# Kernel tuning notes

Hardware: AMD Instinct MI355X
Metric: run time of the kernel (lower is better)

Reference implementation:

```python
import jax, jax.numpy as jnp
import numpy as np

B, C, H, W = 4, 64, 224, 224
WS = 14
HEADS = 4
HD = C // HEADS  # 16
N = WS * WS      # 196
SCALE = HD ** -0.5


def conv2d(x, w, b, pad):
    y = jax.lax.conv_general_dilated(x, w, (1, 1), [(pad, pad), (pad, pad)],
                                     dimension_numbers=('NCHW', 'OIHW', 'NCHW'))
    return y + b[None, :, None, None]


def layernorm(x, g, b, eps=1e-5):
    m = jnp.mean(x, axis=-1, keepdims=True)
    v = jnp.mean((x - m) ** 2, axis=-1, keepdims=True)
    return (x - m) * jax.lax.rsqrt(v + eps) * g + b


def window_partition(x):
    # x: (B,H,W,C) -> (B*nW, WS, WS, C)
    b, h, w, c = x.shape
    x = x.reshape(b, h // WS, WS, w // WS, WS, c)
    return x.transpose(0, 1, 3, 2, 4, 5).reshape(-1, WS, WS, c)


def window_reverse(win, h, w):
    b = win.shape[0] // ((h // WS) * (w // WS))
    x = win.reshape(b, h // WS, w // WS, WS, WS, -1)
    return x.transpose(0, 1, 3, 2, 4, 5).reshape(b, h, w, -1)


def setup_inputs():
    key = jax.random.key(0)
    ks = iter(jax.random.split(key, 64))
    nrm = lambda shp, s=0.02: (jax.random.normal(next(ks), shp, jnp.float32) * s)
    d = {}
    d['x'] = jax.random.normal(next(ks), (B, C, H, W), jnp.float32)
    d['x_basic'] = jax.random.normal(next(ks), (B, C, H, W), jnp.float32)
    # Aware_offset convs
    d['c1_w'] = nrm((64, 64, 3, 3)); d['c1_b'] = jnp.zeros((64,), jnp.float32)
    d['c2_w'] = nrm((64, 64, 5, 5)); d['c2_b'] = jnp.zeros((64,), jnp.float32)
    d['c3_w'] = nrm((64, 64, 7, 7)); d['c3_b'] = jnp.zeros((64,), jnp.float32)
    d['c4_w'] = nrm((64, 192, 3, 3)); d['c4_b'] = jnp.zeros((64,), jnp.float32)
    d['c5_w'] = nrm((128, 128, 3, 3)); d['c5_b'] = jnp.zeros((128,), jnp.float32)
    d['c6_w'] = nrm((128, 128, 3, 3)); d['c6_b'] = jnp.zeros((128,), jnp.float32)
    d['c7_w'] = nrm((64, 128, 1, 1)); d['c7_b'] = jnp.zeros((64,), jnp.float32)
    d['c8_w'] = nrm((64, 128, 1, 1)); d['c8_b'] = jnp.zeros((64,), jnp.float32)
    # block params
    d['qkv1_w'] = nrm((64, 64, 3, 3)); d['qkv1_b'] = jnp.zeros((64,), jnp.float32)
    d['n1_g'] = jnp.ones((C,), jnp.float32); d['n1_b'] = jnp.zeros((C,), jnp.float32)
    d['qkv_w'] = nrm((3 * C, C)); d['qkv_b'] = jnp.zeros((3 * C,), jnp.float32)
    d['corr_w'] = nrm((N, HD)); d['corr_b'] = jnp.zeros((N,), jnp.float32)
    d['proj_w'] = nrm((C, C)); d['proj_b'] = jnp.zeros((C,), jnp.float32)
    d['n2_g'] = jnp.ones((C,), jnp.float32); d['n2_b'] = jnp.zeros((C,), jnp.float32)
    d['fc1_w'] = nrm((2 * C, C)); d['fc1_b'] = jnp.zeros((2 * C,), jnp.float32)
    d['fc2_w'] = nrm((C, 2 * C)); d['fc2_b'] = jnp.zeros((C,), jnp.float32)
    return d


def _forward(x, x_basic, c1_w, c1_b, c2_w, c2_b, c3_w, c3_b, c4_w, c4_b,
             c5_w, c5_b, c6_w, c6_b, c7_w, c7_b, c8_w, c8_b,
             qkv1_w, qkv1_b, n1_g, n1_b, qkv_w, qkv_b, corr_w, corr_b,
             proj_w, proj_b, n2_g, n2_b, fc1_w, fc1_b, fc2_w, fc2_b):
    relu = jax.nn.relu
    # ---- Aware_offset ----
    in1 = relu(conv2d(x, c1_w, c1_b, 1))
    in2 = relu(conv2d(x, c2_w, c2_b, 2))
    in3 = relu(conv2d(x, c3_w, c3_b, 3))
    xo = relu(conv2d(jnp.concatenate([in1, in2, in3], 1), c4_w, c4_b, 1))
    cat12 = jnp.concatenate([x, x_basic], 1)
    b1 = relu(conv2d(cat12, c5_w, c5_b, 1))
    b2 = jax.nn.sigmoid(relu(conv2d(b1, c6_w, c6_b, 1)))
    b1 = relu(conv2d(b1 * b2, c7_w, c7_b, 0))
    xb = xo * b1 + relu(conv2d(cat12, c8_w, c8_b, 0))  # (B,C,H,W)
    xb = xb.transpose(0, 2, 3, 1)                       # (B,H,W,C)
    # ---- pre-attn: norm1 + convQKV1 ----
    xt = x.reshape(B, C, H * W).transpose(0, 2, 1)      # (B,L,C)
    xt = layernorm(xt, n1_g, n1_b)
    xc = xt.reshape(B, H, W, C).transpose(0, 3, 1, 2)
    xc = conv2d(xc, qkv1_w, qkv1_b, 1).transpose(0, 2, 3, 1)  # (B,H,W,C)
    # ---- windows ----
    xw = window_partition(xc).reshape(-1, N, C)   # (B_,N,C)
    xbw = window_partition(xb).reshape(-1, N, C)
    B_ = xw.shape[0]
    # ---- window attention with correction bias ----
    qkv = (xw @ qkv_w.T + qkv_b).reshape(B_, N, 3, HEADS, HD).transpose(2, 0, 3, 1, 4)
    q, k, v = qkv[0] * SCALE, qkv[1], qkv[2]            # (B_,h,N,hd)
    xcorr = xbw.reshape(B_, N, HEADS, HD).transpose(0, 2, 1, 3)
    xcorr = xcorr @ corr_w.T + corr_b                   # (B_,h,N,196)
    attn = jax.nn.softmax(jnp.einsum('bhnd,bhmd->bhnm', q, k) + xcorr, axis=-1)
    out = jnp.einsum('bhnm,bhmd->bhnd', attn, v).transpose(0, 2, 1, 3).reshape(B_, N, C)
    out = out @ proj_w.T + proj_b
    # ---- reverse + MLP ----
    sx = window_reverse(out.reshape(-1, WS, WS, C), H, W)  # (B,H,W,C)
    xt = sx.reshape(B, H * W, C)
    h = layernorm(xt, n2_g, n2_b)
    h = jax.nn.gelu(h @ fc1_w.T + fc1_b, approximate=False) @ fc2_w.T + fc2_b
    xt = xt + h
    return xt.reshape(B, H, W, C).transpose(0, 3, 1, 2)


def reference(x, x_basic, c1_w, c1_b, c2_w, c2_b, c3_w, c3_b, c4_w, c4_b,
              c5_w, c5_b, c6_w, c6_b, c7_w, c7_b, c8_w, c8_b,
              qkv1_w, qkv1_b, n1_g, n1_b, qkv_w, qkv_b, corr_w, corr_b,
              proj_w, proj_b, n2_g, n2_b, fc1_w, fc1_b, fc2_w, fc2_b):
    return _forward(x, x_basic, c1_w, c1_b, c2_w, c2_b, c3_w, c3_b, c4_w, c4_b,
                    c5_w, c5_b, c6_w, c6_b, c7_w, c7_b, c8_w, c8_b,
                    qkv1_w, qkv1_b, n1_g, n1_b, qkv_w, qkv_b, corr_w, corr_b,
                    proj_w, proj_b, n2_g, n2_b, fc1_w, fc1_b, fc2_w, fc2_b)
```

## Files before the change

### kernel.cpp

```cpp
#include <hip/hip_runtime.h>
#include <hip/hip_bf16.h>
#include <math.h>


#define HW  50176
#define WID 224

typedef unsigned short ushortT;
typedef __attribute__((ext_vector_type(8))) short bf8_t;
typedef __attribute__((ext_vector_type(4))) short bf4_t;
typedef __attribute__((ext_vector_type(4))) float f4_t;

__device__ __forceinline__ ushortT f2bf(float v) {
    __hip_bfloat16 h = __float2bfloat16(v);
    ushortT u; __builtin_memcpy(&u, &h, 2); return u;
}
__device__ __forceinline__ float bf2f(ushortT h) {
    union { float f; unsigned int u; } c; c.u = ((unsigned int)h) << 16;
    return c.f;
}
__device__ __forceinline__ void cvt8(const float* xv, bf8_t& hh, bf8_t& ll) {
    #pragma unroll
    for (int i = 0; i < 8; ++i) {
        ushortT hi = f2bf(xv[i]);
        hh[i] = (short)hi;
        ll[i] = (short)f2bf(xv[i] - bf2f(hi));
    }
}

__global__ __launch_bounds__(256) void packw(
    const float* __restrict__ w, ushortT* __restrict__ dst,
    int K, int IC, int OC, int total)
{
    int e = blockIdx.x * 256 + threadIdx.x;
    if (e >= total) return;
    int KK = K * K;
    int kk = e % KK; int rem = e / KK;
    int ic = rem % IC; int oc = rem / IC;
    float v = w[e];
    ushortT hi = f2bf(v);
    ushortT lo = f2bf(v - bf2f(hi));
    int g = oc >> 6, oc64 = oc & 63;
    int ic32 = ic >> 5, icin = ic & 31, kb = icin >> 3, ii = icin & 7;
    int nch = KK * (IC / 32);
    int chunk = ic32 * KK + kk;
    size_t base = ((size_t)(g * nch + chunk)) * 4096;
    dst[base + (kb * 64 + oc64) * 8 + ii] = hi;
    dst[base + 2048 + (kb * 64 + oc64) * 8 + ii] = lo;
}

__global__ __launch_bounds__(256) void packa32(
    const float* __restrict__ w, ushortT* __restrict__ dst, int K, int total)
{
    int e = blockIdx.x * 256 + threadIdx.x;
    if (e >= total) return;
    int f = e >> 9, r = e & 511, ln = r >> 3, i = r & 7;
    int nk = K >> 5;
    int o = f / nk, ks = f % nk;
    int c = ln & 15, gg = ln >> 4;
    float v = w[(size_t)(o * 16 + c) * K + ks * 32 + gg * 8 + i];
    ushortT hi = f2bf(v);
    dst[(size_t)f * 1024 + ln * 8 + i] = hi;
    dst[(size_t)f * 1024 + 512 + ln * 8 + i] = f2bf(v - bf2f(hi));
}

__global__ __launch_bounds__(256) void packa16(
    const float* __restrict__ w, ushortT* __restrict__ dst, int K, int total)
{
    int e = blockIdx.x * 256 + threadIdx.x;
    if (e >= total) return;
    int f = e >> 8, r = e & 255, ln = r >> 2, i = r & 3;
    int nk = K >> 4;
    int o = f / nk, n = f % nk;
    int c = ln & 15, gg = ln >> 4;
    float v = w[(size_t)(o * 16 + c) * K + n * 16 + gg * 4 + i];
    ushortT hi = f2bf(v);
    dst[(size_t)f * 512 + ln * 4 + i] = hi;
    dst[(size_t)f * 512 + 256 + ln * 4 + i] = f2bf(v - bf2f(hi));
}

template<int K>
__device__ __forceinline__ void convpass(
    const ushortT* __restrict__ wq, const ushortT* __restrict__ sm,
    int wv, int lc, int kb, f4_t (&ac)[2][4])
{
    constexpr int off = 3 - K / 2;
    constexpr int INSH = 14 * 22 * 40;
    const int boff = (kb * 64 + lc) * 8;
    bf8_t bh[4], bl[4];
    #pragma unroll
    for (int n = 0; n < 4; ++n) {
        bh[n] = *(const bf8_t*)(wq + boff + n * 128);
        bl[n] = *(const bf8_t*)(wq + 2048 + boff + n * 128);
    }
    #pragma unroll 1
    for (int kk = 0; kk < K * K; ++kk) {
        bf8_t cbh[4], cbl[4];
        #pragma unroll
        for (int n = 0; n < 4; ++n) { cbh[n] = bh[n]; cbl[n] = bl[n]; }
        if (kk + 1 < K * K) {
            const ushortT* wn = wq + (size_t)(kk + 1) * 4096;
            #pragma unroll
            for (int n = 0; n < 4; ++n) {
                bh[n] = *(const bf8_t*)(wn + boff + n * 128);
                bl[n] = *(const bf8_t*)(wn + 2048 + boff + n * 128);
            }
        }
        const int ky = kk / K, kx = kk % K;
        #pragma unroll
        for (int m = 0; m < 2; ++m) {
            const int row = 2 * wv + m + ky + off;
            const int col = lc + kx + off;
            const ushortT* ab = sm + (row * 22 + col) * 40 + kb * 8;
            bf8_t Ah = *(const bf8_t*)ab;
            bf8_t Al = *(const bf8_t*)(ab + INSH);
            #pragma unroll
            for (int n = 0; n < 4; ++n) {
                ac[m][n] = __builtin_amdgcn_mfma_f32_16x16x32_bf16(Ah, cbh[n], ac[m][n], 0, 0, 0);
                ac[m][n] = __builtin_amdgcn_mfma_f32_16x16x32_bf16(Ah, cbl[n], ac[m][n], 0, 0, 0);
                ac[m][n] = __builtin_amdgcn_mfma_f32_16x16x32_bf16(Al, cbh[n], ac[m][n], 0, 0, 0);
            }
        }
    }
}

__global__ __launch_bounds__(256, 4) void mfconv3(
    const float* __restrict__ in,
    const ushortT* __restrict__ w1p, const ushortT* __restrict__ w2p,
    const ushortT* __restrict__ w3p,
    const float* __restrict__ b1, const float* __restrict__ b2,
    const float* __restrict__ b3,
    float* __restrict__ out, int inStride, int outStride)
{
    constexpr int TWd = 22, THd = 14, ICP = 40;
    constexpr int INSH = THd * TWd * ICP;
    constexpr int E = THd * TWd * 32;
    __shared__ __align__(16) ushortT smem_u[2 * INSH];
    float* pool = (float*)smem_u;

    const int t = threadIdx.x, lane = t & 63, wv = t >> 6;
    const int lc = lane & 15, kb = lane >> 4;
    const int img = blockIdx.z;
    const int x0 = blockIdx.x * 16, y0 = blockIdx.y * 8;
    const float* inb = in + (size_t)img * inStride;

    f4_t acc1[2][4], acc2[2][4], acc3[2][4];
    {
        #pragma unroll
        for (int n = 0; n < 4; ++n) {
            float z1 = b1[n * 16 + lc], z2 = b2[n * 16 + lc], z3 = b3[n * 16 + lc];
            #pragma unroll
            for (int m = 0; m < 2; ++m) {
                acc1[m][n] = (f4_t){z1, z1, z1, z1};
                acc2[m][n] = (f4_t){z2, z2, z2, z2};
                acc3[m][n] = (f4_t){z3, z3, z3, z3};
            }
        }
    }

    #pragma unroll 1
    for (int ic32 = 0; ic32 < 2; ++ic32) {
        __syncthreads();
        #pragma unroll 1
        for (int ib = 0; ib < E; ib += 1024) {
            float v[4];
            #pragma unroll
            for (int u = 0; u < 4; ++u) {
                int i = ib + u * 256 + t;
                v[u] = 0.f;
                if (i < E) {
                    int icn = i / (THd * TWd);
                    int px  = i % (THd * TWd);
                    int ty = px / TWd, tx = px % TWd;
                    int gy = y0 + ty - 3, gx = x0 + tx - 3;
                    if (gy >= 0 && gy < WID && gx >= 0 && gx < WID)
                        v[u] = inb[(size_t)(ic32 * 32 + icn) * HW + gy * WID + gx];
                }
            }
            #pragma unroll
            for (int u = 0; u < 4; ++u) {
                int i = ib + u * 256 + t;
                if (i < E) {
                    int icn = i / (THd * TWd);
                    int px  = i % (THd * TWd);
                    ushortT hi = f2bf(v[u]);
                    smem_u[px * ICP + icn] = hi;
                    smem_u[INSH + px * ICP + icn] = f2bf(v[u] - bf2f(hi));
                }
            }
        }
        __syncthreads();
        convpass<3>(w1p + (size_t)(ic32 *  9) * 4096, smem_u, wv, lc, kb, acc1);
        convpass<5>(w2p + (size_t)(ic32 * 25) * 4096, smem_u, wv, lc, kb, acc2);
        convpass<7>(w3p + (size_t)(ic32 * 49) * 4096, smem_u, wv, lc, kb, acc3);
    }

    #pragma unroll 1
    for (int c = 0; c < 3; ++c) {
        float* ob0 = out + (size_t)img * outStride + (size_t)(c * 64) * HW;
        #pragma unroll
        for (int m = 0; m < 2; ++m) {
            __syncthreads();
            #pragma unroll
            for (int n = 0; n < 4; ++n)
                #pragma unroll
                for (int j = 0; j < 4; ++j) {
                    float v = (c == 0) ? acc1[m][n][j] : (c == 1) ? acc2[m][n][j] : acc3[m][n][j];
                    v = fmaxf(v, 0.f);
                    pool[(wv * 64 + n * 16 + lc) * 20 + kb * 4 + j] = v;
                }
            __syncthreads();
            {
                int rho = t >> 6, oc = t & 63;
                int y = y0 + 2 * rho + m;
                float* ob = ob0 + (size_t)oc * HW + (size_t)y * WID + x0;
                const float* pr = &pool[(rho * 64 + oc) * 20];
                #pragma unroll
                for (int c4 = 0; c4 < 4; ++c4) {
                    float4 st = { pr[c4*4+0], pr[c4*4+1], pr[c4*4+2], pr[c4*4+3] };
                    *(float4*)&ob[c4 * 4] = st;
                }
            }
        }
    }
}

template<int K, int IC, int OC, int ACT, bool CAT, bool LNRM, bool NHWCOUT>
__global__ __launch_bounds__(256, 4) void mfconv(
    const float* __restrict__ in, const float* __restrict__ in2,
    const ushortT* __restrict__ wpk, const float* __restrict__ bias,
    const float* __restrict__ mu, const float* __restrict__ rs,
    const float* __restrict__ lng, const float* __restrict__ lnb,
    float* __restrict__ out, int inStride, int outStride)
{
    constexpr int P = K / 2, TWd = 16 + K - 1, THd = 8 + K - 1, ICP = 40;
    constexpr int OCG = OC / 64, KK = K * K, NCH = KK * (IC / 32);
    constexpr int INSH = THd * TWd * ICP;
    constexpr int E = THd * TWd * 32;
    constexpr int SMU = (2 * INSH > 10240) ? 2 * INSH : 10240;
    __shared__ __align__(16) ushortT smem_u[SMU];
    float* pool = (float*)smem_u;

    const int t = threadIdx.x, lane = t & 63, wv = t >> 6;
    const int lc = lane & 15, kb = lane >> 4;
    const int img = blockIdx.z / OCG, g = blockIdx.z % OCG;
    const int x0 = blockIdx.x * 16, y0 = blockIdx.y * 8;
    const float* inb  = in + (size_t)img * inStride;
    const float* in2b = CAT ? (in2 + (size_t)img * inStride) : nullptr;
    const int imgPixBase = img * HW;
    const ushortT* wq0 = wpk + (size_t)g * NCH * 4096;

    f4_t acc[2][4];
    {
        float bz0 = bias[g * 64 +  0 + lc];
        float bz1 = bias[g * 64 + 16 + lc];
        float bz2 = bias[g * 64 + 32 + lc];
        float bz3 = bias[g * 64 + 48 + lc];
        #pragma unroll
        for (int m = 0; m < 2; ++m) {
            acc[m][0] = (f4_t){bz0, bz0, bz0, bz0};
            acc[m][1] = (f4_t){bz1, bz1, bz1, bz1};
            acc[m][2] = (f4_t){bz2, bz2, bz2, bz2};
            acc[m][3] = (f4_t){bz3, bz3, bz3, bz3};
        }
    }
    const int aoff = lc * ICP + kb * 8;
    const int boff = (kb * 64 + lc) * 8;

    #pragma unroll 1
    for (int ic32 = 0; ic32 < IC / 32; ++ic32) {
        __syncthreads();
        #pragma unroll 1
        for (int ib = 0; ib < E; ib += 1024) {
            float v[4];
            #pragma unroll
            for (int u = 0; u < 4; ++u) {
                int i = ib + u * 256 + t;
                v[u] = 0.f;
                if (i < E) {
                    int icn = i / (THd * TWd);
                    int px  = i % (THd * TWd);
                    int ty = px / TWd, tx = px % TWd;
                    int gy = y0 + ty - P, gx = x0 + tx - P;
                    int ic = ic32 * 32 + icn;
                    if (gy >= 0 && gy < WID && gx >= 0 && gx < WID) {
                        const float* s;
                        if (CAT) s = (ic < 64) ? (inb + (size_t)ic * HW)
                                               : (in2b + (size_t)(ic - 64) * HW);
                        else     s = inb + (size_t)ic * HW;
                        float vv = s[gy * WID + gx];
                        if (LNRM) {
                            int p = imgPixBase + gy * WID + gx;
                            vv = (vv - mu[p]) * rs[p] * lng[ic] + lnb[ic];
                        }
                        v[u] = vv;
                    }
                }
            }
            #pragma unroll
            for (int u = 0; u < 4; ++u) {
                int i = ib + u * 256 + t;
                if (i < E) {
                    int icn = i / (THd * TWd);
                    int px  = i % (THd * TWd);
                    ushortT hi = f2bf(v[u]);
                    smem_u[px * ICP + icn] = hi;
                    smem_u[INSH + px * ICP + icn] = f2bf(v[u] - bf2f(hi));
                }
            }
        }
        __syncthreads();
        const ushortT* wqb = wq0 + (size_t)(ic32 * KK) * 4096;
        bf8_t bh[4], bl[4];
        #pragma unroll
        for (int n = 0; n < 4; ++n) {
            bh[n] = *(const bf8_t*)(wqb + boff + n * 128);
            bl[n] = *(const bf8_t*)(wqb + 2048 + boff + n * 128);
        }
        #pragma unroll 1
        for (int kk = 0; kk < KK; ++kk) {
            bf8_t cbh[4], cbl[4];
            #pragma unroll
            for (int n = 0; n < 4; ++n) { cbh[n] = bh[n]; cbl[n] = bl[n]; }
            if (kk + 1 < KK) {
                const ushortT* wn = wqb + (size_t)(kk + 1) * 4096;
                #pragma unroll
                for (int n = 0; n < 4; ++n) {
                    bh[n] = *(const bf8_t*)(wn + boff + n * 128);
                    bl[n] = *(const bf8_t*)(wn + 2048 + boff + n * 128);
                }
            }
            const int ky = kk / K, kx = kk % K;
            #pragma unroll
            for (int m = 0; m < 2; ++m) {
                const int row = 2 * wv + m + ky;
                const ushortT* ab = smem_u + (row * TWd + kx) * ICP + aoff;
                bf8_t Ah = *(const bf8_t*)ab;
                bf8_t Al = *(const bf8_t*)(ab + INSH);
                #pragma unroll
                for (int n = 0; n < 4; ++n) {
                    acc[m][n] = __builtin_amdgcn_mfma_f32_16x16x32_bf16(Ah, cbh[n], acc[m][n], 0, 0, 0);
                    acc[m][n] = __builtin_amdgcn_mfma_f32_16x16x32_bf16(Ah, cbl[n], acc[m][n], 0, 0, 0);
                    acc[m][n] = __builtin_amdgcn_mfma_f32_16x16x32_bf16(Al, cbh[n], acc[m][n], 0, 0, 0);
                }
            }
        }
    }
    if (NHWCOUT) {
        float* ob0 = out + (size_t)img * outStride;
        #pragma unroll
        for (int m = 0; m < 2; ++m) {
            __syncthreads();
            #pragma unroll
            for (int n = 0; n < 4; ++n)
                #pragma unroll
                for (int j = 0; j < 4; ++j) {
                    float v = acc[m][n][j];
                    if (ACT == 1) v = fmaxf(v, 0.f);
                    else if (ACT == 2) v = 1.f / (1.f + __expf(-fmaxf(v, 0.f)));
                    pool[(wv * 16 + kb * 4 + j) * 68 + n * 16 + lc] = v;
                }
            __syncthreads();
            {
                int pix = t >> 2, q = t & 3;
                int y = y0 + 2 * (pix >> 4) + m;
                int x = x0 + (pix & 15);
                float* pr = ob0 + ((size_t)y * WID + x) * 64 + q * 16;
                const float* src = &pool[pix * 68 + q * 16];
                #pragma unroll
                for (int u = 0; u < 4; ++u)
                    *(float4*)&pr[u * 4] = *(const float4*)&src[u * 4];
            }
        }
    } else {
        float* ob0 = out + (size_t)img * outStride + (size_t)(g * 64) * HW;
        #pragma unroll
        for (int m = 0; m < 2; ++m) {
            __syncthreads();
            #pragma unroll
            for (int n = 0; n < 4; ++n)
                #pragma unroll
                for (int j = 0; j < 4; ++j) {
                    float v = acc[m][n][j];
                    if (ACT == 1) v = fmaxf(v, 0.f);
                    else if (ACT == 2) v = 1.f / (1.f + __expf(-fmaxf(v, 0.f)));
                    pool[(wv * 64 + n * 16 + lc) * 20 + kb * 4 + j] = v;
                }
            __syncthreads();
            {
                int rho = t >> 6, oc = t & 63;
                int y = y0 + 2 * rho + m;
                float* ob = ob0 + (size_t)oc * HW + (size_t)y * WID + x0;
                const float* pr = &pool[(rho * 64 + oc) * 20];
                #pragma unroll
                for (int c4 = 0; c4 < 4; ++c4) {
                    float4 st = { pr[c4*4+0], pr[c4*4+1], pr[c4*4+2], pr[c4*4+3] };
                    *(float4*)&ob[c4 * 4] = st;
                }
            }
        }
    }
}

__global__ __launch_bounds__(256) void ln_stats(
    const float* __restrict__ x, float* __restrict__ mu, float* __restrict__ rs)
{
    const int p = blockIdx.x * 256 + threadIdx.x;
    const int img = p / HW, pp = p - img * HW;
    const float* b = x + (size_t)img * 64 * HW + pp;
    float row[64];
    #pragma unroll
    for (int c = 0; c < 64; ++c) row[c] = b[(size_t)c * HW];
    float s1 = 0.f;
    #pragma unroll
    for (int c = 0; c < 64; ++c) s1 += row[c];
    float m = s1 * (1.f / 64.f);
    float s2 = 0.f;
    #pragma unroll
    for (int c = 0; c < 64; ++c) { float d = row[c] - m; s2 += d * d; }
    mu[p] = m;
    rs[p] = rsqrtf(s2 * (1.f / 64.f) + 1e-5f);
}

__global__ __launch_bounds__(256) void xb1x1(
    const float* __restrict__ x, const float* __restrict__ xbas,
    const float* __restrict__ xo, const float* __restrict__ b1, const float* __restrict__ b2,
    const float* __restrict__ c7w, const float* __restrict__ c7b,
    const float* __restrict__ c8w, const float* __restrict__ c8b,
    float* __restrict__ xbout)
{
    __shared__ __align__(16) float w7s[128 * 36], w8s[128 * 36];
    const int t = threadIdx.x, oh = blockIdx.y;
    for (int i = t; i < 4096; i += 256) {
        int o = i >> 7, ic = i & 127;
        w7s[ic * 36 + o] = c7w[(size_t)(oh * 32 + o) * 128 + ic];
        w8s[ic * 36 + o] = c8w[(size_t)(oh * 32 + o) * 128 + ic];
    }
    __syncthreads();
    const int p = blockIdx.x * 256 + t;
    const int img = p / HW, pp = p - img * HW;
    const float* b1p = b1 + (size_t)img * 128 * HW + pp;
    const float* b2p = b2 + (size_t)img * 128 * HW + pp;
    const float* xp  = x  + (size_t)img * 64 * HW + pp;
    const float* xbp = xbas + (size_t)img * 64 * HW + pp;
    float a7[32], a8[32];
    {
        const float4* c74 = (const float4*)(c7b + oh * 32);
        const float4* c84 = (const float4*)(c8b + oh * 32);
        #pragma unroll
        for (int j4 = 0; j4 < 8; ++j4) {
            float4 v7 = c74[j4], v8 = c84[j4];
            a7[j4*4+0]=v7.x; a7[j4*4+1]=v7.y; a7[j4*4+2]=v7.z; a7[j4*4+3]=v7.w;
            a8[j4*4+0]=v8.x; a8[j4*4+1]=v8.y; a8[j4*4+2]=v8.z; a8[j4*4+3]=v8.w;
        }
    }
    #pragma unroll 4
    for (int ic = 0; ic < 128; ++ic) {
        float tv = b1p[(size_t)ic * HW] * b2p[(size_t)ic * HW];
        float cv = (ic < 64) ? xp[(size_t)ic * HW] : xbp[(size_t)(ic - 64) * HW];
        const float4* w7r = (const float4*)&w7s[ic * 36];
        const float4* w8r = (const float4*)&w8s[ic * 36];
        #pragma unroll
        for (int j4 = 0; j4 < 8; ++j4) {
            float4 v7 = w7r[j4], v8 = w8r[j4];
            a7[j4*4+0] = fmaf(tv, v7.x, a7[j4*4+0]);
            a7[j4*4+1] = fmaf(tv, v7.y, a7[j4*4+1]);
            a7[j4*4+2] = fmaf(tv, v7.z, a7[j4*4+2]);
            a7[j4*4+3] = fmaf(tv, v7.w, a7[j4*4+3]);
            a8[j4*4+0] = fmaf(cv, v8.x, a8[j4*4+0]);
            a8[j4*4+1] = fmaf(cv, v8.y, a8[j4*4+1]);
            a8[j4*4+2] = fmaf(cv, v8.z, a8[j4*4+2]);
            a8[j4*4+3] = fmaf(cv, v8.w, a8[j4*4+3]);
        }
    }
    const float* xop = xo + (size_t)img * 64 * HW + pp;
    float* orow = xbout + (size_t)p * 64 + oh * 32;
    #pragma unroll
    for (int j4 = 0; j4 < 8; ++j4) {
        float4 st;
        st.x = xop[(size_t)(oh*32 + j4*4+0) * HW] * fmaxf(a7[j4*4+0], 0.f) + fmaxf(a8[j4*4+0], 0.f);
        st.y = xop[(size_t)(oh*32 + j4*4+1) * HW] * fmaxf(a7[j4*4+1], 0.f) + fmaxf(a8[j4*4+1], 0.f);
        st.z = xop[(size_t)(oh*32 + j4*4+2) * HW] * fmaxf(a7[j4*4+2], 0.f) + fmaxf(a8[j4*4+2], 0.f);
        st.w = xop[(size_t)(oh*32 + j4*4+3) * HW] * fmaxf(a7[j4*4+3], 0.f) + fmaxf(a8[j4*4+3], 0.f);
        *(float4*)&orow[j4 * 4] = st;
    }
}

__global__ __launch_bounds__(256) void attn(
    const float* __restrict__ xc, const float* __restrict__ xb,
    const float* __restrict__ qkvw, const float* __restrict__ qkvb,
    const float* __restrict__ corw, const float* __restrict__ corb,
    float* __restrict__ aout)
{
    constexpr int QS = 40;
    constexpr int VS = 212;
    __shared__ __align__(16) ushortT Kth[196 * QS];
    __shared__ __align__(16) ushortT Ktl[196 * QS];
    __shared__ __align__(16) ushortT Vth[16 * VS];
    __shared__ __align__(16) ushortT Vtl[16 * VS];
    __shared__ __align__(16) float CB[208];

    const int t = threadIdx.x;
    const int wdw = blockIdx.x >> 2, h = blockIdx.x & 3;
    const int b = wdw >> 8, wl = wdw & 255;
    const int wy = (wl >> 4) * 14, wx = (wl & 15) * 14;
    const int lane = t & 63, wv = t >> 6;
    const int g = lane >> 4, col = lane & 15;

    bf8_t Wqh[2], Wql[2], Wkh[2], Wkl[2], Wvh[2], Wvl[2];
    float qb[4], kb[4], vb[4];
    {
        #pragma unroll
        for (int ks = 0; ks < 2; ++ks) {
            float xv[8];
            const float* wr = qkvw + (h * 16 + col) * 64 + ks * 32 + g * 8;
            *(float4*)&xv[0] = *(const float4*)wr;
            *(float4*)&xv[4] = *(const float4*)(wr + 4);
            cvt8(xv, Wqh[ks], Wql[ks]);
            wr = qkvw + (64 + h * 16 + col) * 64 + ks * 32 + g * 8;
            *(float4*)&xv[0] = *(const float4*)wr;
            *(float4*)&xv[4] = *(const float4*)(wr + 4);
            cvt8(xv, Wkh[ks], Wkl[ks]);
            wr = qkvw + (128 + h * 16 + col) * 64 + ks * 32 + g * 8;
            *(float4*)&xv[0] = *(const float4*)wr;
            *(float4*)&xv[4] = *(const float4*)(wr + 4);
            cvt8(xv, Wvh[ks], Wvl[ks]);
        }
        float4 q4 = *(const float4*)(qkvb + h * 16 + g * 4);
        float4 k4 = *(const float4*)(qkvb + 64 + h * 16 + g * 4);
        float4 v4 = *(const float4*)(qkvb + 128 + h * 16 + g * 4);
        qb[0]=q4.x; qb[1]=q4.y; qb[2]=q4.z; qb[3]=q4.w;
        kb[0]=k4.x; kb[1]=k4.y; kb[2]=k4.z; kb[3]=k4.w;
        vb[0]=v4.x; vb[1]=v4.y; vb[2]=v4.z; vb[3]=v4.w;
    }

    if (t < 208) CB[t] = (t < 196) ? corb[t] : 0.f;
    if (t < 196) {
        unsigned* khr = (unsigned*)&Kth[t * QS];
        unsigned* klr = (unsigned*)&Ktl[t * QS];
        float xw[16];
        const float4* cw4 = (const float4*)(corw + t * 16);
        #pragma unroll
        for (int j = 0; j < 4; ++j) *(float4*)&xw[j * 4] = cw4[j];
        #pragma unroll
        for (int i = 0; i < 8; ++i) {
            ushortT ah = f2bf(xw[2*i]), bh = f2bf(xw[2*i+1]);
            ushortT al = f2bf(xw[2*i] - bf2f(ah)), bl = f2bf(xw[2*i+1] - bf2f(bh));
            khr[8 + i] = (unsigned)ah | ((unsigned)bh << 16);
            klr[8 + i] = (unsigned)al | ((unsigned)bl << 16);
        }
    }

    auto phaseB = [&](int mt) -> f4_t {
        const int row = 16 * mt + col;
        const int pix = (row > 195) ? 195 : row;
        const int rr = pix / 14, cc = pix - (pix / 14) * 14;
        const float* xr = xc + (size_t)((b * 224 + wy + rr) * 224 + wx + cc) * 64;
        f4_t dq = (f4_t){0.f, 0.f, 0.f, 0.f};
        f4_t dk = (f4_t){0.f, 0.f, 0.f, 0.f};
        f4_t dv = (f4_t){0.f, 0.f, 0.f, 0.f};
        #pragma unroll
        for (int ks = 0; ks < 2; ++ks) {
            float xv[8];
            *(float4*)&xv[0] = *(const float4*)(xr + ks * 32 + g * 8);
            *(float4*)&xv[4] = *(const float4*)(xr + ks * 32 + g * 8 + 4);
            bf8_t Xh, Xl;
            cvt8(xv, Xh, Xl);
            dq = __builtin_amdgcn_mfma_f32_16x16x32_bf16(Wqh[ks], Xh, dq, 0, 0, 0);
            dq = __builtin_amdgcn_mfma_f32_16x16x32_bf16(Wqh[ks], Xl, dq, 0, 0, 0);
            dq = __builtin_amdgcn_mfma_f32_16x16x32_bf16(Wql[ks], Xh, dq, 0, 0, 0);
            dk = __builtin_amdgcn_mfma_f32_16x16x32_bf16(Wkh[ks], Xh, dk, 0, 0, 0);
            dk = __builtin_amdgcn_mfma_f32_16x16x32_bf16(Wkh[ks], Xl, dk, 0, 0, 0);
            dk = __builtin_amdgcn_mfma_f32_16x16x32_bf16(Wkl[ks], Xh, dk, 0, 0, 0);
            dv = __builtin_amdgcn_mfma_f32_16x16x32_bf16(Wvh[ks], Xh, dv, 0, 0, 0);
            dv = __builtin_amdgcn_mfma_f32_16x16x32_bf16(Wvh[ks], Xl, dv, 0, 0, 0);
            dv = __builtin_amdgcn_mfma_f32_16x16x32_bf16(Wvl[ks], Xh, dv, 0, 0, 0);
        }
        #pragma unroll
        for (int j = 0; j < 4; ++j) {
            float v = dv[j] + vb[j];
            ushortT hi = f2bf(v);
            Vth[(g * 4 + j) * VS + row] = hi;
            Vtl[(g * 4 + j) * VS + row] = f2bf(v - bf2f(hi));
        }
        if (row < 196) {
            unsigned h0, h1, l0, l1;
            {
                float a = dk[0] + kb[0], bb = dk[1] + kb[1];
                ushortT ah = f2bf(a), bh = f2bf(bb);
                h0 = (unsigned)ah | ((unsigned)bh << 16);
                l0 = (unsigned)f2bf(a - bf2f(ah)) | ((unsigned)f2bf(bb - bf2f(bh)) << 16);
            }
            {
                float a = dk[2] + kb[2], bb = dk[3] + kb[3];
                ushortT ah = f2bf(a), bh = f2bf(bb);
                h1 = (unsigned)ah | ((unsigned)bh << 16);
                l1 = (unsigned)f2bf(a - bf2f(ah)) | ((unsigned)f2bf(bb - bf2f(bh)) << 16);
            }
            uint2 u;
            u.x = h0; u.y = h1; *(uint2*)&Kth[row * QS + g * 4] = u;
            u.x = l0; u.y = l1; *(uint2*)&Ktl[row * QS + g * 4] = u;
        }
        return (f4_t){(dq[0] + qb[0]) * 0.25f, (dq[1] + qb[1]) * 0.25f,
                      (dq[2] + qb[2]) * 0.25f, (dq[3] + qb[3]) * 0.25f};
    };

    f4_t dqs0 = phaseB(wv);
    f4_t dqs1 = phaseB(wv + 4);
    f4_t dqs2 = phaseB(wv + 8);
    f4_t dqs3 = (f4_t){0.f, 0.f, 0.f, 0.f};
    if (wv == 0) dqs3 = phaseB(12);
    __syncthreads();

    auto phaseC = [&](f4_t dqv, int qt) {
        const int row = 16 * qt + col;
        const int pixq = (row > 195) ? 195 : row;
        float q8[8];
        const int sl0 = ((2 * g) & 3) * 16 + col;
        const int sl1 = ((2 * g + 1) & 3) * 16 + col;
        q8[0] = __shfl(dqv[0], sl0); q8[1] = __shfl(dqv[1], sl0);
        q8[2] = __shfl(dqv[2], sl0); q8[3] = __shfl(dqv[3], sl0);
        q8[4] = __shfl(dqv[0], sl1); q8[5] = __shfl(dqv[1], sl1);
        q8[6] = __shfl(dqv[2], sl1); q8[7] = __shfl(dqv[3], sl1);
        if (g >= 2) {
            const int rr = pixq / 14, cc = pixq - (pixq / 14) * 14;
            const float* xr = xb + (size_t)((b * 224 + wy + rr) * 224 + wx + cc) * 64
                            + h * 16 + (g & 1) * 8;
            *(float4*)&q8[0] = *(const float4*)xr;
            *(float4*)&q8[4] = *(const float4*)(xr + 4);
        }
        bf8_t Bhf, Blf;
        cvt8(q8, Bhf, Blf);
        f4_t s[13];
        __builtin_amdgcn_s_setprio(1);
        #pragma unroll
        for (int kt = 0; kt < 13; ++kt) {
            const int krow = (16 * kt + col > 195) ? 195 : (16 * kt + col);
            const bf8_t Ahf = *(const bf8_t*)&Kth[krow * QS + g * 8];
            const bf8_t Alf = *(const bf8_t*)&Ktl[krow * QS + g * 8];
            f4_t a = (f4_t){0.f, 0.f, 0.f, 0.f};
            a = __builtin_amdgcn_mfma_f32_16x16x32_bf16(Ahf, Bhf, a, 0, 0, 0);
            a = __builtin_amdgcn_mfma_f32_16x16x32_bf16(Ahf, Blf, a, 0, 0, 0);
            a = __builtin_amdgcn_mfma_f32_16x16x32_bf16(Alf, Bhf, a, 0, 0, 0);
            const f4_t cb4 = *(const f4_t*)&CB[16 * kt + g * 4];
            s[kt] = a + cb4;
        }
        __builtin_amdgcn_s_setprio(0);
        if (g > 0) { s[12][0] = -3e38f; s[12][1] = -3e38f; s[12][2] = -3e38f; s[12][3] = -3e38f; }
        float mrow = -3e38f;
        #pragma unroll
        for (int kt = 0; kt < 13; ++kt)
            #pragma unroll
            for (int j = 0; j < 4; ++j) mrow = fmaxf(mrow, s[kt][j]);
        mrow = fmaxf(mrow, __shfl_xor(mrow, 16));
        mrow = fmaxf(mrow, __shfl_xor(mrow, 32));
        float lsum = 0.f;
        bf4_t ph[13], pl[13];
        #pragma unroll
        for (int kt = 0; kt < 13; ++kt) {
            #pragma unroll
            for (int j = 0; j < 4; ++j) {
                float p = __expf(s[kt][j] - mrow);
                lsum += p;
                ushortT hi = f2bf(p);
                ph[kt][j] = (short)hi;
                pl[kt][j] = (short)f2bf(p - bf2f(hi));
            }
        }
        lsum += __shfl_xor(lsum, 16);
        lsum += __shfl_xor(lsum, 32);
        f4_t o = (f4_t){0.f, 0.f, 0.f, 0.f};
        __builtin_amdgcn_s_setprio(1);
        #pragma unroll
        for (int kt = 0; kt < 13; ++kt) {
            const bf4_t vh = *(const bf4_t*)&Vth[col * VS + 16 * kt + g * 4];
            const bf4_t vl = *(const bf4_t*)&Vtl[col * VS + 16 * kt + g * 4];
            o = __builtin_amdgcn_mfma_f32_16x16x16bf16_1k(vh, ph[kt], o, 0, 0, 0);
            o = __builtin_amdgcn_mfma_f32_16x16x16bf16_1k(vl, ph[kt], o, 0, 0, 0);
            o = __builtin_amdgcn_mfma_f32_16x16x16bf16_1k(vh, pl[kt], o, 0, 0, 0);
        }
        __builtin_amdgcn_s_setprio(0);
        const int pix = 16 * qt + col;
        if (pix < 196) {
            const float inv = 1.f / lsum;
            const int rr = pix / 14, cc = pix % 14;
            const size_t pixIdx = (size_t)((b * 224 + wy + rr) * 224 + wx + cc);
            float4 st = { o[0] * inv, o[1] * inv, o[2] * inv, o[3] * inv };
            *(float4*)&aout[pixIdx * 64 + h * 16 + g * 4] = st;
        }
    };

    phaseC(dqs0, wv);
    phaseC(dqs1, wv + 4);
    phaseC(dqs2, wv + 8);
    if (wv == 0) phaseC(dqs3, 12);
}

__global__ __launch_bounds__(256) void mlpmf(
    const float* __restrict__ aout, const ushortT* __restrict__ pk,
    const float* __restrict__ pbias,
    const float* __restrict__ lng, const float* __restrict__ lnb,
    const float* __restrict__ fc1b, const float* __restrict__ fc2b,
    float* __restrict__ out)
{
    const int t = threadIdx.x, lane = t & 63, wv = t >> 6;
    const int gq = lane >> 4, col = lane & 15;
    const int p0 = (blockIdx.x * 4 + wv) * 16;
    const ushortT* pk1 = pk;
    const ushortT* pk2 = pk + 8192;
    const ushortT* pk3 = pk + 24576;

    f4_t S[4];
    #pragma unroll
    for (int n = 0; n < 4; ++n) {
        float4 b4 = *(const float4*)(pbias + n * 16 + gq * 4);
        S[n] = (f4_t){b4.x, b4.y, b4.z, b4.w};
    }
    const float* xr = aout + (size_t)(p0 + col) * 64;
    #pragma unroll
    for (int ks = 0; ks < 2; ++ks) {
        float xv[8];
        *(float4*)&xv[0] = *(const float4*)(xr + ks * 32 + gq * 8);
        *(float4*)&xv[4] = *(const float4*)(xr + ks * 32 + gq * 8 + 4);
        bf8_t Xh, Xl;
        cvt8(xv, Xh, Xl);
        #pragma unroll
        for (int n = 0; n < 4; ++n) {
            const ushortT* a = pk1 + (size_t)(n * 2 + ks) * 1024 + lane * 8;
            bf8_t Ah = *(const bf8_t*)a;
            bf8_t Al = *(const bf8_t*)(a + 512);
            S[n] = __builtin_amdgcn_mfma_f32_16x16x32_bf16(Ah, Xh, S[n], 0, 0, 0);
            S[n] = __builtin_amdgcn_mfma_f32_16x16x32_bf16(Ah, Xl, S[n], 0, 0, 0);
            S[n] = __builtin_amdgcn_mfma_f32_16x16x32_bf16(Al, Xh, S[n], 0, 0, 0);
        }
    }
    float sum = 0.f;
    #pragma unroll
    for (int n = 0; n < 4; ++n)
        #pragma unroll
        for (int j = 0; j < 4; ++j) sum += S[n][j];
    sum += __shfl_xor(sum, 16);
    sum += __shfl_xor(sum, 32);
    float mean = sum * (1.f / 64.f);
    float var = 0.f;
    #pragma unroll
    for (int n = 0; n < 4; ++n)
        #pragma unroll
        for (int j = 0; j < 4; ++j) { float d = S[n][j] - mean; var += d * d; }
    var += __shfl_xor(var, 16);
    var += __shfl_xor(var, 32);
    float rstd = rsqrtf(var * (1.f / 64.f) + 1e-5f);
    bf4_t Nh[4], Nl[4];
    #pragma unroll
    for (int n = 0; n < 4; ++n) {
        float4 g4 = *(const float4*)(lng + n * 16 + gq * 4);
        float4 b4 = *(const float4*)(lnb + n * 16 + gq * 4);
        float nv0 = (S[n][0] - mean) * rstd * g4.x + b4.x;
        float nv1 = (S[n][1] - mean) * rstd * g4.y + b4.y;
        float nv2 = (S[n][2] - mean) * rstd * g4.z + b4.z;
        float nv3 = (S[n][3] - mean) * rstd * g4.w + b4.w;
        ushortT h0 = f2bf(nv0), h1 = f2bf(nv1), h2 = f2bf(nv2), h3 = f2bf(nv3);
        Nh[n][0] = (short)h0; Nh[n][1] = (short)h1; Nh[n][2] = (short)h2; Nh[n][3] = (short)h3;
        Nl[n][0] = (short)f2bf(nv0 - bf2f(h0));
        Nl[n][1] = (short)f2bf(nv1 - bf2f(h1));
        Nl[n][2] = (short)f2bf(nv2 - bf2f(h2));
        Nl[n][3] = (short)f2bf(nv3 - bf2f(h3));
    }
    bf4_t Gh[8], Gl[8];
    #pragma unroll
    for (int o = 0; o < 8; ++o) {
        float4 b4 = *(const float4*)(fc1b + o * 16 + gq * 4);
        f4_t hacc = (f4_t){b4.x, b4.y, b4.z, b4.w};
        #pragma unroll
        for (int n = 0; n < 4; ++n) {
            const ushortT* a = pk2 + (size_t)(o * 4 + n) * 512 + lane * 4;
            bf4_t Ah = *(const bf4_t*)a;
            bf4_t Al = *(const bf4_t*)(a + 256);
            hacc = __builtin_amdgcn_mfma_f32_16x16x16bf16_1k(Ah, Nh[n], hacc, 0, 0, 0);
            hacc = __builtin_amdgcn_mfma_f32_16x16x16bf16_1k(Ah, Nl[n], hacc, 0, 0, 0);
            hacc = __builtin_amdgcn_mfma_f32_16x16x16bf16_1k(Al, Nh[n], hacc, 0, 0, 0);
        }
        #pragma unroll
        for (int j = 0; j < 4; ++j) {
            float hv = hacc[j];
            float gl = 0.5f * hv * (1.f + erff(hv * 0.70710678118f));
            ushortT hi = f2bf(gl);
            Gh[o][j] = (short)hi;
            Gl[o][j] = (short)f2bf(gl - bf2f(hi));
        }
    }
    const int img = p0 / HW, pp = p0 - img * HW;
    float* ob = out + (size_t)img * 64 * HW + pp + col;
    #pragma unroll
    for (int o2 = 0; o2 < 4; ++o2) {
        float4 b4 = *(const float4*)(fc2b + o2 * 16 + gq * 4);
        f4_t oacc = (f4_t){b4.x, b4.y, b4.z, b4.w};
        #pragma unroll
        for (int k2 = 0; k2 < 8; ++k2) {
            const ushortT* a = pk3 + (size_t)(o2 * 8 + k2) * 512 + lane * 4;
            bf4_t Ah = *(const bf4_t*)a;
            bf4_t Al = *(const bf4_t*)(a + 256);
            oacc = __builtin_amdgcn_mfma_f32_16x16x16bf16_1k(Ah, Gh[k2], oacc, 0, 0, 0);
            oacc = __builtin_amdgcn_mfma_f32_16x16x16bf16_1k(Ah, Gl[k2], oacc, 0, 0, 0);
            oacc = __builtin_amdgcn_mfma_f32_16x16x16bf16_1k(Al, Gh[k2], oacc, 0, 0, 0);
        }
        #pragma unroll
        for (int j = 0; j < 4; ++j) {
            int och = o2 * 16 + gq * 4 + j;
            ob[(size_t)och * HW] = S[o2][j] + oacc[j];
        }
    }
}

extern "C" void kernel_launch(void* const* d_in, const int* in_sizes, int n_in,
                              void* d_out, int out_size, void* d_ws, size_t ws_size,
                              hipStream_t stream)
{
    (void)in_sizes; (void)n_in; (void)out_size;
    const float* x      = (const float*)d_in[0];
    const float* xbasic = (const float*)d_in[1];
    const float* c1w  = (const float*)d_in[2];  const float* c1b  = (const float*)d_in[3];
    const float* c2w  = (const float*)d_in[4];  const float* c2b  = (const float*)d_in[5];
    const float* c3w  = (const float*)d_in[6];  const float* c3b  = (const float*)d_in[7];
    const float* c4w  = (const float*)d_in[8];  const float* c4b  = (const float*)d_in[9];
    const float* c5w  = (const float*)d_in[10]; const float* c5b  = (const float*)d_in[11];
    const float* c6w  = (const float*)d_in[12]; const float* c6b  = (const float*)d_in[13];
    const float* c7w  = (const float*)d_in[14]; const float* c7b  = (const float*)d_in[15];
    const float* c8w  = (const float*)d_in[16]; const float* c8b  = (const float*)d_in[17];
    const float* qk1w = (const float*)d_in[18]; const float* qk1b = (const float*)d_in[19];
    const float* n1g  = (const float*)d_in[20]; const float* n1b  = (const float*)d_in[21];
    const float* qkvw = (const float*)d_in[22]; const float* qkvb = (const float*)d_in[23];
    const float* corw = (const float*)d_in[24]; const float* corb = (const float*)d_in[25];
    const float* prjw = (const float*)d_in[26]; const float* prjb = (const float*)d_in[27];
    const float* n2g  = (const float*)d_in[28]; const float* n2b  = (const float*)d_in[29];
    const float* f1w  = (const float*)d_in[30]; const float* f1b  = (const float*)d_in[31];
    const float* f2w  = (const float*)d_in[32]; const float* f2b  = (const float*)d_in[33];

    float* ws = (float*)d_ws;
    const size_t SCR0 = 26836992ull;
    const size_t need4 = (SCR0 + 4ull * 19267584ull) * 4ull;
    const size_t need2 = (SCR0 + 2ull * 19267584ull) * 4ull;
    const int CS = (ws_size >= need4) ? 4 : (ws_size >= need2) ? 2 : 1;
    const int nch = 4 / CS;

    float* XC = ws;
    float* XB = ws + 12845056;
    float* MU = ws + 25690112;
    float* RS = ws + 25890816;
    ushortT* WP = (ushortT*)(ws + 26091520);
    float* A  = ws + SCR0;
    float* XO = A + (size_t)CS * 9633792;
    float* B1 = XO + (size_t)CS * 3211264;
    float* B2 = A;
    float* AOUT = A;
    ushortT* WQ1 = (ushortT*)B1;
    ushortT* PM  = (ushortT*)MU;

    const size_t o1 = 0, o2 = 73728, o3 = 278528, o4 = 679936, o5 = 901120, o6 = 1196032;

    ln_stats<<<784, 256, 0, stream>>>(x, MU, RS);

    {
        auto PK = [&](const float* w, ushortT* dst, int K, int IC, int OC) {
            int tot = OC * IC * K * K;
            packw<<<(tot + 255) / 256, 256, 0, stream>>>(w, dst, K, IC, OC, tot);
        };
        PK(qk1w, WQ1, 3, 64, 64);
        PK(c1w, WP + o1, 3, 64, 64);
        PK(c2w, WP + o2, 5, 64, 64);
        PK(c3w, WP + o3, 7, 64, 64);
        PK(c4w, WP + o4, 3, 192, 64);
        PK(c5w, WP + o5, 3, 128, 128);
        PK(c6w, WP + o6, 3, 128, 128);
    }

    mfconv<3, 64, 64, 0, false, true, true><<<dim3(14, 28, 4), 256, 0, stream>>>(
        x, nullptr, WQ1, qk1b, MU, RS, n1g, n1b, XC, 64 * HW, HW * 64);

    packa32<<<16, 256, 0, stream>>>(prjw, PM, 64, 4096);
    packa16<<<32, 256, 0, stream>>>(f1w, PM + 8192, 64, 8192);
    packa16<<<32, 256, 0, stream>>>(f2w, PM + 24576, 128, 8192);

    for (int ch = 0; ch < nch; ++ch) {
        const float* xi  = x      + (size_t)ch * CS * 64 * HW;
        const float* xbi = xbasic + (size_t)ch * CS * 64 * HW;
        mfconv3<<<dim3(14, 28, CS), 256, 0, stream>>>(
            xi, WP + o1, WP + o2, WP + o3, c1b, c2b, c3b, A, 64 * HW, 192 * HW);
        mfconv<3, 192, 64, 1, false, false, false><<<dim3(14, 28, CS), 256, 0, stream>>>(
            A, nullptr, WP + o4, c4b, nullptr, nullptr, nullptr, nullptr, XO, 192 * HW, 64 * HW);
        mfconv<3, 128, 128, 1, true, false, false><<<dim3(14, 28, CS * 2), 256, 0, stream>>>(
            xi, xbi, WP + o5, c5b, nullptr, nullptr, nullptr, nullptr, B1, 64 * HW, 128 * HW);
        mfconv<3, 128, 128, 2, false, false, false><<<dim3(14, 28, CS * 2), 256, 0, stream>>>(
            B1, nullptr, WP + o6, c6b, nullptr, nullptr, nullptr, nullptr, B2, 128 * HW, 128 * HW);
        xb1x1<<<dim3(CS * 196, 2), 256, 0, stream>>>(
            xi, xbi, XO, B1, B2, c7w, c7b, c8w, c8b, XB + (size_t)ch * CS * HW * 64);
    }

    attn<<<4096, 256, 0, stream>>>(XC, XB, qkvw, qkvb, corw, corb, AOUT);
    mlpmf<<<3136, 256, 0, stream>>>(AOUT, PM, prjb, n2g, n2b, f1b, f2b,
                                    (float*)d_out);
}
```

Measured before the change: 1.778 ms.

## Split mfconv3 work across 8 waves with one output row each

The fused 3/5/7 conv kernel now launches 512 threads per block, with each wave computing a single output row instead of two. This halves the accumulator registers per thread and doubles the waves per block, aiming for more latency hiding and occupancy. In exchange, every wave reloads the full weight fragments for only half the MFMA work, which doubles weight-load traffic per MFMA.

```diff
diff --git a/kernel.cpp b/kernel.cpp
--- a/kernel.cpp
+++ b/kernel.cpp
@@ -80,9 +80,9 @@
 }
 
 template<int K>
-__device__ __forceinline__ void convpass(
+__device__ __forceinline__ void convpass8(
     const ushortT* __restrict__ wq, const ushortT* __restrict__ sm,
-    int wv, int lc, int kb, f4_t (&ac)[2][4])
+    int wv, int lc, int kb, f4_t (&ac)[4])
 {
     constexpr int off = 3 - K / 2;
     constexpr int INSH = 14 * 22 * 40;
@@ -107,24 +107,21 @@
             }
         }
         const int ky = kk / K, kx = kk % K;
-        #pragma unroll
-        for (int m = 0; m < 2; ++m) {
-            const int row = 2 * wv + m + ky + off;
-            const int col = lc + kx + off;
-            const ushortT* ab = sm + (row * 22 + col) * 40 + kb * 8;
-            bf8_t Ah = *(const bf8_t*)ab;
-            bf8_t Al = *(const bf8_t*)(ab + INSH);
-            #pragma unroll
-            for (int n = 0; n < 4; ++n) {
-                ac[m][n] = __builtin_amdgcn_mfma_f32_16x16x32_bf16(Ah, cbh[n], ac[m][n], 0, 0, 0);
-                ac[m][n] = __builtin_amdgcn_mfma_f32_16x16x32_bf16(Ah, cbl[n], ac[m][n], 0, 0, 0);
-                ac[m][n] = __builtin_amdgcn_mfma_f32_16x16x32_bf16(Al, cbh[n], ac[m][n], 0, 0, 0);
-            }
-        }
-    }
-}
-
-__global__ __launch_bounds__(256, 4) void mfconv3(
+        const int row = wv + ky + off;
+        const int col = lc + kx + off;
+        const ushortT* ab = sm + (row * 22 + col) * 40 + kb * 8;
+        bf8_t Ah = *(const bf8_t*)ab;
+        bf8_t Al = *(const bf8_t*)(ab + INSH);
+        #pragma unroll
+        for (int n = 0; n < 4; ++n) {
+            ac[n] = __builtin_amdgcn_mfma_f32_16x16x32_bf16(Ah, cbh[n], ac[n], 0, 0, 0);
+            ac[n] = __builtin_amdgcn_mfma_f32_16x16x32_bf16(Ah, cbl[n], ac[n], 0, 0, 0);
+            ac[n] = __builtin_amdgcn_mfma_f32_16x16x32_bf16(Al, cbh[n], ac[n], 0, 0, 0);
+        }
+    }
+}
+
+__global__ __launch_bounds__(512) void mfconv3(
     const float* __restrict__ in,
     const ushortT* __restrict__ w1p, const ushortT* __restrict__ w2p,
     const ushortT* __restrict__ w3p,
@@ -144,29 +141,24 @@
     const int x0 = blockIdx.x * 16, y0 = blockIdx.y * 8;
     const float* inb = in + (size_t)img * inStride;
 
-    f4_t acc1[2][4], acc2[2][4], acc3[2][4];
-    {
-        #pragma unroll
-        for (int n = 0; n < 4; ++n) {
-            float z1 = b1[n * 16 + lc], z2 = b2[n * 16 + lc], z3 = b3[n * 16 + lc];
-            #pragma unroll
-            for (int m = 0; m < 2; ++m) {
-                acc1[m][n] = (f4_t){z1, z1, z1, z1};
-                acc2[m][n] = (f4_t){z2, z2, z2, z2};
-                acc3[m][n] = (f4_t){z3, z3, z3, z3};
-            }
-        }
+    f4_t acc1[4], acc2[4], acc3[4];
+    #pragma unroll
+    for (int n = 0; n < 4; ++n) {
+        float z1 = b1[n * 16 + lc], z2 = b2[n * 16 + lc], z3 = b3[n * 16 + lc];
+        acc1[n] = (f4_t){z1, z1, z1, z1};
+        acc2[n] = (f4_t){z2, z2, z2, z2};
+        acc3[n] = (f4_t){z3, z3, z3, z3};
     }
 
     #pragma unroll 1
     for (int ic32 = 0; ic32 < 2; ++ic32) {
         __syncthreads();
         #pragma unroll 1
-        for (int ib = 0; ib < E; ib += 1024) {
+        for (int ib = 0; ib < E; ib += 2048) {
             float v[4];
             #pragma unroll
             for (int u = 0; u < 4; ++u) {
-                int i = ib + u * 256 + t;
+                int i = ib + u * 512 + t;
                 v[u] = 0.f;
                 if (i < E) {
                     int icn = i / (THd * TWd);
@@ -179,7 +171,7 @@
             }
             #pragma unroll
             for (int u = 0; u < 4; ++u) {
-                int i = ib + u * 256 + t;
+                int i = ib + u * 512 + t;
                 if (i < E) {
                     int icn = i / (THd * TWd);
                     int px  = i % (THd * TWd);
@@ -190,36 +182,33 @@
             }
         }
         __syncthreads();
-        convpass<3>(w1p + (size_t)(ic32 *  9) * 4096, smem_u, wv, lc, kb, acc1);
-        convpass<5>(w2p + (size_t)(ic32 * 25) * 4096, smem_u, wv, lc, kb, acc2);
-        convpass<7>(w3p + (size_t)(ic32 * 49) * 4096, smem_u, wv, lc, kb, acc3);
+        convpass8<3>(w1p + (size_t)(ic32 *  9) * 4096, smem_u, wv, lc, kb, acc1);
+        convpass8<5>(w2p + (size_t)(ic32 * 25) * 4096, smem_u, wv, lc, kb, acc2);
+        convpass8<7>(w3p + (size_t)(ic32 * 49) * 4096, smem_u, wv, lc, kb, acc3);
     }
 
     #pragma unroll 1
     for (int c = 0; c < 3; ++c) {
         float* ob0 = out + (size_t)img * outStride + (size_t)(c * 64) * HW;
-        #pragma unroll
-        for (int m = 0; m < 2; ++m) {
-            __syncthreads();
-            #pragma unroll
-            for (int n = 0; n < 4; ++n)
-                #pragma unroll
-                for (int j = 0; j < 4; ++j) {
-                    float v = (c == 0) ? acc1[m][n][j] : (c == 1) ? acc2[m][n][j] : acc3[m][n][j];
-                    v = fmaxf(v, 0.f);
-                    pool[(wv * 64 + n * 16 + lc) * 20 + kb * 4 + j] = v;
-                }
-            __syncthreads();
-            {
-                int rho = t >> 6, oc = t & 63;
-                int y = y0 + 2 * rho + m;
-                float* ob = ob0 + (size_t)oc * HW + (size_t)y * WID + x0;
-                const float* pr = &pool[(rho * 64 + oc) * 20];
-                #pragma unroll
-                for (int c4 = 0; c4 < 4; ++c4) {
-                    float4 st = { pr[c4*4+0], pr[c4*4+1], pr[c4*4+2], pr[c4*4+3] };
-                    *(float4*)&ob[c4 * 4] = st;
-                }
+        __syncthreads();
+        #pragma unroll
+        for (int n = 0; n < 4; ++n)
+            #pragma unroll
+            for (int j = 0; j < 4; ++j) {
+                float v = (c == 0) ? acc1[n][j] : (c == 1) ? acc2[n][j] : acc3[n][j];
+                v = fmaxf(v, 0.f);
+                pool[(wv * 64 + n * 16 + lc) * 20 + kb * 4 + j] = v;
+            }
+        __syncthreads();
+        {
+            int rho = t >> 6, oc = t & 63;
+            int y = y0 + rho;
+            float* ob = ob0 + (size_t)oc * HW + (size_t)y * WID + x0;
+            const float* pr = &pool[(rho * 64 + oc) * 20];
+            #pragma unroll
+            for (int c4 = 0; c4 < 4; ++c4) {
+                float4 st = { pr[c4*4+0], pr[c4*4+1], pr[c4*4+2], pr[c4*4+3] };
+                *(float4*)&ob[c4 * 4] = st;
             }
         }
     }
@@ -884,7 +873,7 @@
     for (int ch = 0; ch < nch; ++ch) {
         const float* xi  = x      + (size_t)ch * CS * 64 * HW;
         const float* xbi = xbasic + (size_t)ch * CS * 64 * HW;
-        mfconv3<<<dim3(14, 28, CS), 256, 0, stream>>>(
+        mfconv3<<<dim3(14, 28, CS), 512, 0, stream>>>(
             xi, WP + o1, WP + o2, WP + o3, c1b, c2b, c3b, A, 64 * HW, 192 * HW);
         mfconv<3, 192, 64, 1, false, false, false><<<dim3(14, 28, CS), 256, 0, stream>>>(
             A, nullptr, WP + o4, c4b, nullptr, nullptr, nullptr, nullptr, XO, 192 * HW, 64 * HW);
```

After: 2.043 ms. 1.15x slower.
